# Kernel tuning notes

Measured on AMD Instinct MI355X. Metric: run time of the kernel, lower is better.

## Reference

```python
import jax, jax.numpy as jnp
import numpy as np

N_NODES = 100000
N_EDGES = 800000
F_IN = 64
UNITS = 64


def setup_inputs() -> dict:
    key = jax.random.key(0)
    k1, k2, k3, k4, k5, k6 = jax.random.split(key, 6)
    x = jax.random.normal(k1, (N_NODES, F_IN), dtype=jnp.float32)
    w = jax.random.normal(k2, (F_IN, UNITS), dtype=jnp.float32)
    b = jax.random.normal(k3, (UNITS,), dtype=jnp.float32)
    edge_weight = jax.random.uniform(k4, (N_EDGES,), dtype=jnp.float32)
    edge_row = jax.random.randint(k5, (N_EDGES,), 0, N_NODES, dtype=jnp.int32)
    edge_col = jax.random.randint(k6, (N_EDGES,), 0, N_NODES, dtype=jnp.int32)
    return {"x": x, "w": w, "b": b, "edge_weight": edge_weight,
            "edge_row": edge_row, "edge_col": edge_col}


def reference(x, w, b, edge_weight, edge_row, edge_col):
    # GCN layer: out = A_hat @ (X W) + b, A_hat given in COO form.
    xw = jnp.matmul(x, w)                          # [N, units] dense projection
    msgs = xw[edge_col] * edge_weight[:, None]     # [E, units] gather + scale
    out = jax.ops.segment_sum(msgs, edge_row, num_segments=N_NODES)  # SpMM reduce
    return out + b
```

## Files before the change

### kernel.cpp

```cpp
#include <hip/hip_runtime.h>
#include <hip/hip_fp16.h>

#define N_NODES 100000
#define N_EDGES 800000
#define FDIM 64
#define TILE_ROWS 32
#define N_TILES (N_NODES / TILE_ROWS)
#define SCAN_BLOCK 1024
#define N_SCAN_BLOCKS ((N_NODES + SCAN_BLOCK - 1) / SCAN_BLOCK)
#define ROWS_PER_XCD (N_NODES / 8)

typedef int   iv4 __attribute__((ext_vector_type(4)));
typedef float fv4 __attribute__((ext_vector_type(4)));

__global__ __launch_bounds__(256) void gemm_hist_kernel(
    const float* __restrict__ x, const float* __restrict__ w,
    const int* __restrict__ erow, __half* __restrict__ xwh,
    int* __restrict__ count) {
    const int tid = threadIdx.x;
    const int bid = blockIdx.x;

    const int e = bid * 256 + tid;
    if (e < N_EDGES) atomicAdd(&count[erow[e]], 1);

    __shared__ float wq[16 * 64 * 4];
    __shared__ float xs[TILE_ROWS * FDIM];

    const int lane = tid & 63;
    const int wid = tid >> 6;

    float4* wq4 = reinterpret_cast<float4*>(wq);
    #pragma unroll
    for (int it = 0; it < 4; ++it) {
        const int k0 = wid * 4 + it;
        float4 wv;
        wv.x = w[(4 * k0 + 0) * FDIM + lane];
        wv.y = w[(4 * k0 + 1) * FDIM + lane];
        wv.z = w[(4 * k0 + 2) * FDIM + lane];
        wv.w = w[(4 * k0 + 3) * FDIM + lane];
        wq4[k0 * 64 + lane] = wv;
    }

    {
        const float4* xg4 = reinterpret_cast<const float4*>(
            x + (size_t)bid * TILE_ROWS * FDIM);
        float4* xs4 = reinterpret_cast<float4*>(xs);
        xs4[tid] = xg4[tid];
        xs4[256 + tid] = xg4[256 + tid];
    }
    __syncthreads();

    const float4* xs4 = reinterpret_cast<const float4*>(xs);
    const int rbase = wid * 8;
    float acc[8] = {0.f, 0.f, 0.f, 0.f, 0.f, 0.f, 0.f, 0.f};
    #pragma unroll 4
    for (int k0 = 0; k0 < 16; ++k0) {
        const float4 wv = wq4[k0 * 64 + lane];
        #pragma unroll
        for (int rr = 0; rr < 8; ++rr) {
            const float4 xv = xs4[(rbase + rr) * 16 + k0];
            acc[rr] += xv.x * wv.x + xv.y * wv.y + xv.z * wv.z + xv.w * wv.w;
        }
    }

    const int growbase = bid * TILE_ROWS + rbase;
    #pragma unroll
    for (int rr = 0; rr < 8; ++rr)
        xwh[(size_t)(growbase + rr) * FDIM + lane] = __float2half(acc[rr]);
}

__global__ __launch_bounds__(SCAN_BLOCK) void scan_block_kernel(
    const int* __restrict__ count, int* __restrict__ starts,
    int* __restrict__ blockSums) {
    __shared__ int tmp[SCAN_BLOCK];
    const int tid = threadIdx.x;
    const int i = blockIdx.x * SCAN_BLOCK + tid;
    const int v = (i < N_NODES) ? count[i] : 0;
    tmp[tid] = v;
    __syncthreads();
    for (int off = 1; off < SCAN_BLOCK; off <<= 1) {
        int t = (tid >= off) ? tmp[tid - off] : 0;
        __syncthreads();
        tmp[tid] += t;
        __syncthreads();
    }
    if (i < N_NODES) starts[i] = tmp[tid] - v;
    if (tid == SCAN_BLOCK - 1) blockSums[blockIdx.x] = tmp[tid];
}

__global__ __launch_bounds__(256) void scanadd_kernel(
    int* __restrict__ starts, const int* __restrict__ blockSums,
    int* __restrict__ cursor) {
    __shared__ int ssum[128];
    const int tid = threadIdx.x;
    if (tid < 128) ssum[tid] = (tid < N_SCAN_BLOCKS) ? blockSums[tid] : 0;
    __syncthreads();
    for (int off = 1; off < 128; off <<= 1) {
        int t = (tid < 128 && tid >= off) ? ssum[tid - off] : 0;
        __syncthreads();
        if (tid < 128) ssum[tid] += t;
        __syncthreads();
    }
    const int i = blockIdx.x * 256 + tid;
    if (i < N_NODES) {
        const int j = i >> 10;
        const int add = (j == 0) ? 0 : ssum[j - 1];
        const int s = starts[i] + add;
        starts[i] = s;
        cursor[i] = s;
    } else if (i == N_NODES) {
        starts[N_NODES] = N_EDGES;
    }
}

__global__ __launch_bounds__(256) void fill_xcd_kernel(
    const int* __restrict__ erow, const int* __restrict__ ecol,
    const float* __restrict__ ew, int* __restrict__ cursor,
    uint2* __restrict__ recs) {
    const int xcd = blockIdx.x & 7;
    const int lo = xcd * ROWS_PER_XCD;
    const int hi = lo + ROWS_PER_XCD;
    const int chunk = blockIdx.x >> 3;
    const int base = (chunk * 256 + threadIdx.x) * 4;
    if (base + 3 < N_EDGES) {
        iv4 r = __builtin_nontemporal_load(
            reinterpret_cast<const iv4*>(erow + base));
        iv4 c = __builtin_nontemporal_load(
            reinterpret_cast<const iv4*>(ecol + base));
        fv4 wt = __builtin_nontemporal_load(
            reinterpret_cast<const fv4*>(ew + base));
        #pragma unroll
        for (int j = 0; j < 4; ++j) {
            const int rr = r[j];
            if (rr >= lo && rr < hi) {
                const int p = atomicAdd(&cursor[rr], 1);
                recs[p] = make_uint2((unsigned)c[j], __float_as_uint(wt[j]));
            }
        }
    } else {
        for (int e = base; e < N_EDGES; ++e) {
            const int rr = erow[e];
            if (rr >= lo && rr < hi) {
                const int p = atomicAdd(&cursor[rr], 1);
                recs[p] = make_uint2((unsigned)ecol[e], __float_as_uint(ew[e]));
            }
        }
    }
}

__global__ __launch_bounds__(256) void aggregate_h_kernel(
    const __half* __restrict__ xwh, const uint2* __restrict__ recs,
    const int* __restrict__ starts, const float* __restrict__ b,
    float* __restrict__ out) {
    const int lane = threadIdx.x & 63;
    const int g = lane >> 4;
    const int s = lane & 15;
    const int wave = (int)((blockIdx.x * blockDim.x + threadIdx.x) >> 6);
    const int nwaves = (int)((gridDim.x * (size_t)blockDim.x) >> 6);
    const float4 bias = reinterpret_cast<const float4*>(b)[s];
    const unsigned long long* recs8 =
        reinterpret_cast<const unsigned long long*>(recs);

    for (int r0 = wave * 4; r0 < N_NODES; r0 += nwaves * 4) {
        const int r = r0 + g;
        if (r < N_NODES) {
            const int st = starts[r];
            const int cnt = starts[r + 1] - st;
            float4 acc = bias;
            int k = 0;
            for (; k + 4 <= cnt; k += 4) {
                unsigned long long p0 = __builtin_nontemporal_load(recs8 + st + k + 0);
                unsigned long long p1 = __builtin_nontemporal_load(recs8 + st + k + 1);
                unsigned long long p2 = __builtin_nontemporal_load(recs8 + st + k + 2);
                unsigned long long p3 = __builtin_nontemporal_load(recs8 + st + k + 3);
                uint2 g0 = *reinterpret_cast<const uint2*>(
                    xwh + (size_t)(unsigned)p0 * FDIM + 4 * s);
                uint2 g1 = *reinterpret_cast<const uint2*>(
                    xwh + (size_t)(unsigned)p1 * FDIM + 4 * s);
                uint2 g2 = *reinterpret_cast<const uint2*>(
                    xwh + (size_t)(unsigned)p2 * FDIM + 4 * s);
                uint2 g3 = *reinterpret_cast<const uint2*>(
                    xwh + (size_t)(unsigned)p3 * FDIM + 4 * s);
                const float w0 = __uint_as_float((unsigned)(p0 >> 32));
                const float w1 = __uint_as_float((unsigned)(p1 >> 32));
                const float w2 = __uint_as_float((unsigned)(p2 >> 32));
                const float w3 = __uint_as_float((unsigned)(p3 >> 32));
                float2 a0 = __half22float2(*reinterpret_cast<__half2*>(&g0.x));
                float2 b0 = __half22float2(*reinterpret_cast<__half2*>(&g0.y));
                float2 a1 = __half22float2(*reinterpret_cast<__half2*>(&g1.x));
                float2 b1 = __half22float2(*reinterpret_cast<__half2*>(&g1.y));
                float2 a2 = __half22float2(*reinterpret_cast<__half2*>(&g2.x));
                float2 b2 = __half22float2(*reinterpret_cast<__half2*>(&g2.y));
                float2 a3 = __half22float2(*reinterpret_cast<__half2*>(&g3.x));
                float2 b3 = __half22float2(*reinterpret_cast<__half2*>(&g3.y));
                acc.x += a0.x * w0 + a1.x * w1 + a2.x * w2 + a3.x * w3;
                acc.y += a0.y * w0 + a1.y * w1 + a2.y * w2 + a3.y * w3;
                acc.z += b0.x * w0 + b1.x * w1 + b2.x * w2 + b3.x * w3;
                acc.w += b0.y * w0 + b1.y * w1 + b2.y * w2 + b3.y * w3;
            }
            for (; k < cnt; ++k) {
                unsigned long long p0 = __builtin_nontemporal_load(recs8 + st + k);
                uint2 g0 = *reinterpret_cast<const uint2*>(
                    xwh + (size_t)(unsigned)p0 * FDIM + 4 * s);
                const float w0 = __uint_as_float((unsigned)(p0 >> 32));
                float2 a0 = __half22float2(*reinterpret_cast<__half2*>(&g0.x));
                float2 b0 = __half22float2(*reinterpret_cast<__half2*>(&g0.y));
                acc.x += a0.x * w0; acc.y += a0.y * w0;
                acc.z += b0.x * w0; acc.w += b0.y * w0;
            }
            reinterpret_cast<float4*>(out + (size_t)r * FDIM)[s] = acc;
        }
    }
}

__global__ __launch_bounds__(256) void gemm_rm_kernel(
    const float* __restrict__ x, const float* __restrict__ w,
    float* __restrict__ xw) {
    const int lane = threadIdx.x & 63;
    float wr[FDIM];
    #pragma unroll
    for (int k = 0; k < FDIM; ++k) wr[k] = w[k * FDIM + lane];
    const int gwave = blockIdx.x * 4 + (threadIdx.x >> 6);
    const int nwaves = gridDim.x * 4;
    for (int row = gwave; row < N_NODES; row += nwaves) {
        const float4* xr = reinterpret_cast<const float4*>(x + (size_t)row * FDIM);
        float a0 = 0.f, a1 = 0.f, a2 = 0.f, a3 = 0.f;
        #pragma unroll
        for (int k0 = 0; k0 < FDIM / 4; ++k0) {
            float4 xv = xr[k0];
            a0 += xv.x * wr[4 * k0 + 0];
            a1 += xv.y * wr[4 * k0 + 1];
            a2 += xv.z * wr[4 * k0 + 2];
            a3 += xv.w * wr[4 * k0 + 3];
        }
        xw[(size_t)row * FDIM + lane] = (a0 + a1) + (a2 + a3);
    }
}

__global__ __launch_bounds__(256) void init_out_kernel(
    float* __restrict__ out, const float* __restrict__ b) {
    const float4* b4 = reinterpret_cast<const float4*>(b);
    float4* out4 = reinterpret_cast<float4*>(out);
    const size_t total = (size_t)N_NODES * FDIM / 4;
    size_t i = (size_t)blockIdx.x * blockDim.x + threadIdx.x;
    const size_t stride = (size_t)gridDim.x * blockDim.x;
    for (; i < total; i += stride) out4[i] = b4[i & 15];
}

__global__ __launch_bounds__(256) void scatter_kernel(
    const float* __restrict__ xw, const float* __restrict__ ew,
    const int* __restrict__ erow, const int* __restrict__ ecol,
    float* __restrict__ out) {
    const int lane = threadIdx.x & 63;
    const int g = lane >> 4;
    const int s = lane & 15;
    const int wave = (int)((blockIdx.x * blockDim.x + threadIdx.x) >> 6);
    const int nwaves = (int)((gridDim.x * (size_t)blockDim.x) >> 6);
    for (int e0 = wave * 4; e0 < N_EDGES; e0 += nwaves * 4) {
        const int e = e0 + g;
        if (e < N_EDGES) {
            const int c = ecol[e];
            const int r = erow[e];
            const float wgt = ew[e];
            const float4 v =
                reinterpret_cast<const float4*>(xw + (size_t)c * FDIM)[s];
            float* dst = out + (size_t)r * FDIM + 4 * s;
            atomicAdd(dst + 0, v.x * wgt);
            atomicAdd(dst + 1, v.y * wgt);
            atomicAdd(dst + 2, v.z * wgt);
            atomicAdd(dst + 3, v.w * wgt);
        }
    }
}

extern "C" void kernel_launch(void* const* d_in, const int* in_sizes, int n_in,
                              void* d_out, int out_size, void* d_ws, size_t ws_size,
                              hipStream_t stream) {
    const float* x  = (const float*)d_in[0];
    const float* w  = (const float*)d_in[1];
    const float* b  = (const float*)d_in[2];
    const float* ew = (const float*)d_in[3];
    const int* erow = (const int*)d_in[4];
    const int* ecol = (const int*)d_in[5];
    float* out = (float*)d_out;

    char* ws = (char*)d_ws;
    const size_t XWH_BYTES  = (size_t)N_NODES * FDIM * 2;
    const size_t REC_BYTES  = (size_t)N_EDGES * 8;
    const size_t CNT_BYTES  = (size_t)N_NODES * 4;
    const size_t ST_BYTES   = ((size_t)(N_NODES + 1) * 4 + 15) & ~(size_t)15;
    const size_t SUMS_BYTES = 512;
    const size_t NEED = XWH_BYTES + REC_BYTES + CNT_BYTES + ST_BYTES +
                        CNT_BYTES + SUMS_BYTES;

    if (ws_size >= NEED) {
        __half* xwh    = (__half*)ws;
        uint2* recs    = (uint2*)(ws + XWH_BYTES);
        int* count     = (int*)(ws + XWH_BYTES + REC_BYTES);
        int* starts    = (int*)(ws + XWH_BYTES + REC_BYTES + CNT_BYTES);
        int* cursor    = (int*)(ws + XWH_BYTES + REC_BYTES + CNT_BYTES + ST_BYTES);
        int* blockSums = (int*)(ws + XWH_BYTES + REC_BYTES + CNT_BYTES + ST_BYTES + CNT_BYTES);

        const int gE4 = (N_EDGES / 4 + 255) / 256;
        const int gN  = (N_NODES + 255) / 256 + 1;

        hipMemsetAsync(count, 0, CNT_BYTES, stream);
        gemm_hist_kernel<<<N_TILES, 256, 0, stream>>>(x, w, erow, xwh, count);
        scan_block_kernel<<<N_SCAN_BLOCKS, SCAN_BLOCK, 0, stream>>>(count, starts, blockSums);
        scanadd_kernel<<<gN, 256, 0, stream>>>(starts, blockSums, cursor);
        fill_xcd_kernel<<<gE4 * 8, 256, 0, stream>>>(erow, ecol, ew, cursor, recs);
        aggregate_h_kernel<<<2048, 256, 0, stream>>>(xwh, recs, starts, b, out);
    } else {
        float* xw = (float*)ws;
        gemm_rm_kernel<<<2048, 256, 0, stream>>>(x, w, xw);
        init_out_kernel<<<2048, 256, 0, stream>>>(out, b);
        scatter_kernel<<<2048, 256, 0, stream>>>(xw, ew, erow, ecol, out);
    }
}
```

Baseline: 194.7 us.

## Split histogram from GEMM and build per-XCD LDS histograms

```diff
diff --git a/kernel.cpp b/kernel.cpp
--- a/kernel.cpp
+++ b/kernel.cpp
@@ -9,19 +9,17 @@
 #define SCAN_BLOCK 1024
 #define N_SCAN_BLOCKS ((N_NODES + SCAN_BLOCK - 1) / SCAN_BLOCK)
 #define ROWS_PER_XCD (N_NODES / 8)
+#define HIST_SLICES 16
+#define EDGES_PER_SLICE (N_EDGES / HIST_SLICES)
 
 typedef int   iv4 __attribute__((ext_vector_type(4)));
 typedef float fv4 __attribute__((ext_vector_type(4)));
 
-__global__ __launch_bounds__(256) void gemm_hist_kernel(
+__global__ __launch_bounds__(256) void gemm_kernel(
     const float* __restrict__ x, const float* __restrict__ w,
-    const int* __restrict__ erow, __half* __restrict__ xwh,
-    int* __restrict__ count) {
+    __half* __restrict__ xwh) {
     const int tid = threadIdx.x;
     const int bid = blockIdx.x;
-
-    const int e = bid * 256 + tid;
-    if (e < N_EDGES) atomicAdd(&count[erow[e]], 1);
 
     __shared__ float wq[16 * 64 * 4];
     __shared__ float xs[TILE_ROWS * FDIM];
@@ -67,6 +65,35 @@
     #pragma unroll
     for (int rr = 0; rr < 8; ++rr)
         xwh[(size_t)(growbase + rr) * FDIM + lane] = __float2half(acc[rr]);
+}
+
+__global__ __launch_bounds__(256) void hist_lds_kernel(
+    const int* __restrict__ erow, int* __restrict__ count) {
+    const int xcd = blockIdx.x & 7;
+    const int slice = blockIdx.x >> 3;
+    const int lo = xcd * ROWS_PER_XCD;
+    __shared__ int lhist[ROWS_PER_XCD];
+    for (int i = threadIdx.x; i < ROWS_PER_XCD; i += 256) lhist[i] = 0;
+    __syncthreads();
+
+    const int sbeg = slice * EDGES_PER_SLICE;
+    const int send = sbeg + EDGES_PER_SLICE;
+    for (int e0 = sbeg + threadIdx.x * 4; e0 < send; e0 += 1024) {
+        iv4 r = __builtin_nontemporal_load(
+            reinterpret_cast<const iv4*>(erow + e0));
+        #pragma unroll
+        for (int j = 0; j < 4; ++j) {
+            const int rel = r[j] - lo;
+            if ((unsigned)rel < (unsigned)ROWS_PER_XCD)
+                atomicAdd(&lhist[rel], 1);
+        }
+    }
+    __syncthreads();
+
+    for (int i = threadIdx.x; i < ROWS_PER_XCD; i += 256) {
+        const int v = lhist[i];
+        if (v) atomicAdd(&count[lo + i], v);
+    }
 }
 
 __global__ __launch_bounds__(SCAN_BLOCK) void scan_block_kernel(
@@ -305,7 +332,8 @@
         const int gN  = (N_NODES + 255) / 256 + 1;
 
         hipMemsetAsync(count, 0, CNT_BYTES, stream);
-        gemm_hist_kernel<<<N_TILES, 256, 0, stream>>>(x, w, erow, xwh, count);
+        gemm_kernel<<<N_TILES, 256, 0, stream>>>(x, w, xwh);
+        hist_lds_kernel<<<HIST_SLICES * 8, 256, 0, stream>>>(erow, count);
         scan_block_kernel<<<N_SCAN_BLOCKS, SCAN_BLOCK, 0, stream>>>(count, starts, blockSums);
         scanadd_kernel<<<gN, 256, 0, stream>>>(starts, blockSums, cursor);
         fill_xcd_kernel<<<gE4 * 8, 256, 0, stream>>>(erow, ecol, ew, cursor, recs);
```

Measured after the change: 216.5 us. +11.2%, slower.
